# Optimization experiments

Hardware: AMD Instinct MI355X
Metric: run time of the kernel (lower is better)

## Reference

```python
import jax, jax.numpy as jnp
import numpy as np

N = 32768          # nodes
E = 131072         # edges
H = 4              # heads
RNA = 128          # rna_feature_dim
PROT = 32          # prot_feature_dim
F0 = 64            # num_features_per_layer[0] == [1]
CIN = F0 + PROT    # cross-path feature dim (96)
LRELU = 0.2


def _param(key, shape):
    return jax.random.normal(key, shape, dtype=jnp.float32) * 0.1


def setup_inputs() -> dict:
    key = jax.random.key(0)
    ks = jax.random.split(key, 20)
    return {
        "rna_data": jax.random.normal(ks[0], (N, RNA), dtype=jnp.float32),
        "prot_data": jax.random.normal(ks[1], (N, PROT), dtype=jnp.float32),
        "edge_index": jax.random.randint(ks[2], (2, E), 0, N, dtype=jnp.int32),
        "W_gat_proj": _param(ks[3], (RNA, F0)),
        "b_gat_proj": _param(ks[4], (F0,)),
        "W_gat_reproj": _param(ks[5], (F0, RNA)),
        "b_gat_reproj": _param(ks[6], (RNA,)),
        "Wg": _param(ks[7], (F0, H * F0)),
        "ag_src": _param(ks[8], (H, F0)),
        "ag_trg": _param(ks[9], (H, F0)),
        "bg": _param(ks[10], (F0,)),
        "W_cross_proj": _param(ks[11], (RNA + PROT, CIN)),
        "b_cross_proj": _param(ks[12], (CIN,)),
        "W_cross_reproj": _param(ks[13], (CIN, RNA + PROT)),
        "b_cross_reproj": _param(ks[14], (RNA + PROT,)),
        "Wc": _param(ks[15], (CIN, H * CIN)),
        "ac_src": _param(ks[16], (H, CIN)),
        "ac_trg": _param(ks[17], (H, CIN)),
        "bc": _param(ks[18], (CIN,)),
    }


def gat_layer(x, W, a_src, a_trg, bias, edge_index, softmax_on_src):
    """GATLayer with concat=False, activation=None, skip connection (in==out dim),
    dropout in eval mode. CrossAttnLayer groups the edge-softmax by src instead of trg."""
    n, f = x.shape
    src, trg = edge_index[0], edge_index[1]
    proj = (x @ W).reshape(n, H, f)                               # [N,H,F] lift targets
    s_src = jnp.einsum('nhf,hf->nh', proj, a_src)                 # [N,H]
    s_trg = jnp.einsum('nhf,hf->nh', proj, a_trg)                 # [N,H]
    scores = jax.nn.leaky_relu(s_src[src] + s_trg[trg], LRELU)    # [E,H] per-edge scores
    grp = src if softmax_on_src else trg
    ex = jnp.exp(scores - scores.max())                           # global-max shift (as in source)
    denom = jax.ops.segment_sum(ex, grp, num_segments=n)          # [N,H]
    attn = ex / (denom[grp] + 1e-16)                              # neighborhood-aware softmax [E,H]
    weighted = proj[src] * attn[:, :, None]                       # [E,H,F]
    out = jax.ops.segment_sum(weighted, trg, num_segments=n)      # scatter-add aggregate [N,H,F]
    out = out + x[:, None, :]                                     # direct skip (out_dim == in_dim)
    out = out.mean(axis=1) + bias                                 # concat=False -> head mean, + bias
    return out                                                    # activation=None (last layer)


def reference(rna_data, prot_data, edge_index,
              W_gat_proj, b_gat_proj, W_gat_reproj, b_gat_reproj,
              Wg, ag_src, ag_trg, bg,
              W_cross_proj, b_cross_proj, W_cross_reproj, b_cross_reproj,
              Wc, ac_src, ac_trg, bc):
    concat = jnp.concatenate([rna_data, prot_data], axis=1)       # [N, RNA+PROT]
    rna_p = rna_data @ W_gat_proj + b_gat_proj                    # [N, F0]
    cross_p = concat @ W_cross_proj + b_cross_proj                # [N, CIN]
    gat_out = gat_layer(rna_p, Wg, ag_src, ag_trg, bg, edge_index, False)    # [N, F0]
    cross_out = gat_layer(cross_p, Wc, ac_src, ac_trg, bc, edge_index, True)  # [N, CIN]
    # CrossAttnLayer's trailing view(-1, num_heads, num_out_features)
    cross_out = cross_out.reshape(-1, H, CIN)                     # [N/H, H, CIN]
    gat_final = gat_out @ W_gat_reproj + b_gat_reproj             # [N, RNA]
    cross_final = cross_out @ W_cross_reproj + b_cross_reproj     # [N/H, H, RNA+PROT]
    return gat_final, cross_final
```

## Files before the change

### kernel.cpp

```cpp
#include <hip/hip_runtime.h>
#include <hip/hip_bf16.h>

#define NN 32768
#define NE 131072
#define HH 4

constexpr float kLrelu = 0.2f;

using bf16x8 = __attribute__((ext_vector_type(8))) __bf16;
using f32x4  = __attribute__((ext_vector_type(4))) float;

__device__ inline short f2b(float f) {
    __hip_bfloat16 h = __float2bfloat16(f);
    return __builtin_bit_cast(short, h);
}
__device__ inline float b2f(short s) {
    __hip_bfloat16 h = __builtin_bit_cast(__hip_bfloat16, s);
    return __bfloat162float(h);
}
__device__ inline float blo(int u) {
    return __builtin_bit_cast(float, (int)(u << 16));
}
__device__ inline float bhi(int u) {
    return __builtin_bit_cast(float, (int)(u & 0xffff0000));
}
__device__ inline float lrexp(float x) {
    return __expf(x > 0.f ? x : kLrelu * x);
}

template<int K, int LDA, int OUTN, int BM, int BN, bool BF16OUT>
__global__ __launch_bounds__(256) void mfma_gemm(
    const short* __restrict__ A, const short* __restrict__ Wt,
    const float* __restrict__ bias,
    float* __restrict__ Cf, short* __restrict__ Cb)
{
    constexpr int KP    = K + 8;
    constexpr int WM    = BM / 32;
    constexpr int WN    = 4 / WM;
    constexpr int WBN   = BN / WN;
    constexpr int CF    = WBN / 16;
    constexpr int CPR   = K / 8;
    constexpr int TOT   = (BM + BN) * KP;
    constexpr int SLICE = TOT / 4;

    __shared__ short lds[TOT];
    short* As = lds;
    short* Bs = lds + BM * KP;

    const int tid  = threadIdx.x;
    const int wave = tid >> 6;
    const int lane = tid & 63;
    const int lr   = lane & 15;
    const int kb   = lane >> 4;
    const int wm   = wave % WM;
    const int wn   = wave / WM;
    const int row0 = blockIdx.x * BM;
    const int col0 = blockIdx.y * BN;

    #pragma unroll
    for (int g = tid; g < BM * CPR; g += 256) {
        int r = g / CPR, c = g - r * CPR;
        bf16x8 v = *(const bf16x8*)(A + (size_t)(row0 + r) * LDA + c * 8);
        *(bf16x8*)(As + r * KP + c * 8) = v;
    }
    #pragma unroll
    for (int g = tid; g < BN * CPR; g += 256) {
        int r = g / CPR, c = g - r * CPR;
        bf16x8 v = *(const bf16x8*)(Wt + (size_t)(col0 + r) * K + c * 8);
        *(bf16x8*)(Bs + r * KP + c * 8) = v;
    }
    __syncthreads();

    f32x4 acc[2][CF] = {};
    #pragma unroll
    for (int k0 = 0; k0 < K; k0 += 32) {
        bf16x8 af0 = *(const bf16x8*)(As + (wm * 32 + lr     ) * KP + k0 + kb * 8);
        bf16x8 af1 = *(const bf16x8*)(As + (wm * 32 + lr + 16) * KP + k0 + kb * 8);
        #pragma unroll
        for (int cf = 0; cf < CF; ++cf) {
            bf16x8 bv = *(const bf16x8*)(Bs + (wn * WBN + cf * 16 + lr) * KP + k0 + kb * 8);
            acc[0][cf] = __builtin_amdgcn_mfma_f32_16x16x32_bf16(af0, bv, acc[0][cf], 0, 0, 0);
            acc[1][cf] = __builtin_amdgcn_mfma_f32_16x16x32_bf16(af1, bv, acc[1][cf], 0, 0, 0);
        }
    }

    #pragma unroll
    for (int mf = 0; mf < 2; ++mf) {
        __syncthreads();
        if constexpr (BF16OUT) {
            constexpr int LEP = WBN + 8;
            short* ep = lds + wave * SLICE;
            #pragma unroll
            for (int cf = 0; cf < CF; ++cf) {
                const int c  = cf * 16 + lr;
                const float bv = bias ? bias[col0 + wn * WBN + c] : 0.0f;
                #pragma unroll
                for (int j = 0; j < 4; ++j)
                    ep[(kb * 4 + j) * LEP + c] = f2b(acc[mf][cf][j] + bv);
            }
            __syncthreads();
            constexpr int CROW = WBN / 8;
            for (int g = lane; g < 16 * CROW; g += 64) {
                int r = g / CROW, cc = g - r * CROW;
                bf16x8 v = *(const bf16x8*)(ep + r * LEP + cc * 8);
                *(bf16x8*)(Cb + (size_t)(row0 + wm * 32 + mf * 16 + r) * OUTN
                              + col0 + wn * WBN + cc * 8) = v;
            }
        } else {
            constexpr int LEPF = WBN + 4;
            float* epf = (float*)(lds + wave * SLICE);
            #pragma unroll
            for (int cf = 0; cf < CF; ++cf) {
                const int c  = cf * 16 + lr;
                const float bv = bias ? bias[col0 + wn * WBN + c] : 0.0f;
                #pragma unroll
                for (int j = 0; j < 4; ++j)
                    epf[(kb * 4 + j) * LEPF + c] = acc[mf][cf][j] + bv;
            }
            __syncthreads();
            constexpr int CROWF = WBN / 4;
            for (int g = lane; g < 16 * CROWF; g += 64) {
                int r = g / CROWF, cc = g - r * CROWF;
                float4 v = *(const float4*)(epf + r * LEPF + cc * 4);
                *(float4*)(Cf + (size_t)(row0 + wm * 32 + mf * 16 + r) * OUTN
                              + col0 + wn * WBN + cc * 4) = v;
            }
        }
    }
}

template<int F>
__global__ __launch_bounds__(256) void scores_proj(
    const short* __restrict__ proj_b,
    const float* __restrict__ a_src, const float* __restrict__ a_trg,
    float* __restrict__ ssrc, float* __restrict__ strg)
{
    int t = blockIdx.x * 256 + threadIdx.x;
    if (t >= NN * HH) return;
    int n = t >> 2, h = t & 3;
    const int4* p = (const int4*)(proj_b + (size_t)n * (4 * F) + h * F);
    const float* as = a_src + h * F;
    const float* at = a_trg + h * F;
    float ss = 0.f, st = 0.f;
    #pragma unroll
    for (int c = 0; c < F / 8; ++c) {
        int4 v = p[c];
        int u[4] = { v.x, v.y, v.z, v.w };
        #pragma unroll
        for (int q = 0; q < 4; ++q) {
            float x0 = blo(u[q]), x1 = bhi(u[q]);
            ss += x0 * as[c * 8 + 2 * q] + x1 * as[c * 8 + 2 * q + 1];
            st += x0 * at[c * 8 + 2 * q] + x1 * at[c * 8 + 2 * q + 1];
        }
    }
    ssrc[t] = ss;
    strg[t] = st;
}

__global__ __launch_bounds__(256) void prep_kernel(
    const float* __restrict__ rna, const float* __restrict__ prot,
    short* __restrict__ cb,
    const float* W0, const float* W1, const float* W2,
    const float* W3, const float* W4, const float* W5,
    short* T0, short* T1, short* T2, short* T3, short* T4, short* T5,
    int4* __restrict__ zero_p)
{
    const int bid = blockIdx.x;
    if (bid < 5120) {
        int t = bid * 256 + threadIdx.x;
        int n = t / 40, j = (t - n * 40) * 4;
        float4 v = (j < 128) ? *(const float4*)(rna  + (size_t)n * 128 + j)
                             : *(const float4*)(prot + (size_t)n * 32 + (j - 128));
        short4 o = { f2b(v.x), f2b(v.y), f2b(v.z), f2b(v.w) };
        *(short4*)(cb + (size_t)n * 160 + j) = o;
    } else if (bid < 5984) {
        int idx = bid - 5120;
        int wsel = idx / 144, sub = idx - wsel * 144;
        int K, N; const float* W; short* T;
        switch (wsel) {
            case 0: K = 128; N =  64; W = W0; T = T0; break;
            case 1: K =  64; N = 256; W = W1; T = T1; break;
            case 2: K =  64; N = 128; W = W2; T = T2; break;
            case 3: K = 160; N =  96; W = W3; T = T3; break;
            case 4: K =  96; N = 384; W = W4; T = T4; break;
            default:K =  96; N = 160; W = W5; T = T5; break;
        }
        int t = sub * 256 + threadIdx.x;
        if (t >= K * N) return;
        int n = t / K, k = t - n * K;
        T[t] = f2b(W[(size_t)k * N + n]);
    } else {
        zero_p[(bid - 5984) * 256 + threadIdx.x] = make_int4(0, 0, 0, 0);
    }
}

__global__ __launch_bounds__(256) void hist_dual(const int* __restrict__ ei,
                                                 int* __restrict__ deg_t,
                                                 int* __restrict__ deg_s)
{
    int e = blockIdx.x * 256 + threadIdx.x;
    if (e >= NE) return;
    atomicAdd(&deg_s[ei[e]], 1);
    atomicAdd(&deg_t[ei[NE + e]], 1);
}

__global__ __launch_bounds__(1024) void scan_dual(
    const int* __restrict__ deg_t, int* __restrict__ rowptr_t, int* __restrict__ cursor_t,
    const int* __restrict__ deg_s, int* __restrict__ rowptr_s, int* __restrict__ cursor_s)
{
    const int* deg    = blockIdx.x ? deg_s    : deg_t;
    int*       rowptr = blockIdx.x ? rowptr_s : rowptr_t;
    int*       cursor = blockIdx.x ? cursor_s : cursor_t;
    __shared__ int sums[1024];
    const int t = threadIdx.x;
    const int base = t * 32;
    int local[32];
    int s = 0;
    #pragma unroll
    for (int i = 0; i < 32; ++i) { local[i] = s; s += deg[base + i]; }
    sums[t] = s;
    __syncthreads();
    for (int off = 1; off < 1024; off <<= 1) {
        int v = (t >= off) ? sums[t - off] : 0;
        __syncthreads();
        sums[t] += v;
        __syncthreads();
    }
    const int prev = (t == 0) ? 0 : sums[t - 1];
    #pragma unroll
    for (int i = 0; i < 32; ++i) {
        rowptr[base + i] = prev + local[i];
        cursor[base + i] = prev + local[i];
    }
    if (t == 1023) rowptr[NN] = prev + s;
}

__global__ __launch_bounds__(256) void scatter_dual(
    const int* __restrict__ ei,
    int* __restrict__ cursor_t, int* __restrict__ csr_srcT,
    int* __restrict__ cursor_s, int* __restrict__ csr_trgS)
{
    int e = blockIdx.x * 256 + threadIdx.x;
    if (e >= NE) return;
    int s = ei[e], t = ei[NE + e];
    int st = atomicAdd(&cursor_t[t], 1);
    csr_srcT[st] = s;
    int ss = atomicAdd(&cursor_s[s], 1);
    csr_trgS[ss] = t;
}

__global__ __launch_bounds__(256) void den_src_kernel(
    const int* __restrict__ rowptr_s, const int* __restrict__ csr_trgS,
    const float* __restrict__ ssrc, const float* __restrict__ strg,
    float* __restrict__ recip)
{
    int n = blockIdx.x * 256 + threadIdx.x;
    if (n >= NN) return;
    const int beg = rowptr_s[n], end = rowptr_s[n + 1];
    const float4 sv = *(const float4*)(ssrc + 4 * (size_t)n);
    float d0 = 0.f, d1 = 0.f, d2 = 0.f, d3 = 0.f;
    for (int sl = beg; sl < end; ++sl) {
        const int t = csr_trgS[sl];
        const float4 tv = *(const float4*)(strg + 4 * (size_t)t);
        d0 += lrexp(sv.x + tv.x); d1 += lrexp(sv.y + tv.y);
        d2 += lrexp(sv.z + tv.z); d3 += lrexp(sv.w + tv.w);
    }
    *(float4*)(recip + 4 * (size_t)n) =
        make_float4(1.f / (d0 + 1e-16f), 1.f / (d1 + 1e-16f),
                    1.f / (d2 + 1e-16f), 1.f / (d3 + 1e-16f));
}

template<int F, int NPB, bool GROUP_SRC>
__global__ __launch_bounds__((F / 2) * NPB) void aggregate_fused(
    const int* __restrict__ rowptr_t, const int* __restrict__ csr_srcT,
    const float* __restrict__ ssrc, const float* __restrict__ strg,
    const float* __restrict__ recip,
    const short* __restrict__ proj_b,
    const short* __restrict__ x_pb, const float* __restrict__ bias,
    short* __restrict__ aggb)
{
    const int f2   = threadIdx.x * 2;
    const int node = blockIdx.x * NPB + threadIdx.y;
    const int beg  = rowptr_t[node], end = rowptr_t[node + 1];
    const float4 stv = *(const float4*)(strg + 4 * (size_t)node);

    float a0 = 0.f, a1 = 0.f;
    float h0l = 0.f, h1l = 0.f, h2l = 0.f, h3l = 0.f;
    float h0h = 0.f, h1h = 0.f, h2h = 0.f, h3h = 0.f;
    float d0 = 0.f, d1 = 0.f, d2 = 0.f, d3 = 0.f;

    #pragma unroll 2
    for (int sl = beg; sl < end; ++sl) {
        const int s = csr_srcT[sl];
        const float4 sv = *(const float4*)(ssrc + 4 * (size_t)s);
        float e0 = lrexp(sv.x + stv.x);
        float e1 = lrexp(sv.y + stv.y);
        float e2 = lrexp(sv.z + stv.z);
        float e3 = lrexp(sv.w + stv.w);
        const short* p = proj_b + (size_t)s * (4 * F) + f2;
        const int u0 = *(const int*)(p);
        const int u1 = *(const int*)(p + F);
        const int u2 = *(const int*)(p + 2 * F);
        const int u3 = *(const int*)(p + 3 * F);
        if constexpr (GROUP_SRC) {
            const float4 rc = *(const float4*)(recip + 4 * (size_t)s);
            e0 *= rc.x; e1 *= rc.y; e2 *= rc.z; e3 *= rc.w;
            a0 += e0 * blo(u0) + e1 * blo(u1) + e2 * blo(u2) + e3 * blo(u3);
            a1 += e0 * bhi(u0) + e1 * bhi(u1) + e2 * bhi(u2) + e3 * bhi(u3);
        } else {
            d0 += e0; d1 += e1; d2 += e2; d3 += e3;
            h0l += e0 * blo(u0); h0h += e0 * bhi(u0);
            h1l += e1 * blo(u1); h1h += e1 * bhi(u1);
            h2l += e2 * blo(u2); h2h += e2 * bhi(u2);
            h3l += e3 * blo(u3); h3h += e3 * bhi(u3);
        }
    }
    if constexpr (!GROUP_SRC) {
        const float r0 = 1.f / (d0 + 1e-16f), r1 = 1.f / (d1 + 1e-16f);
        const float r2 = 1.f / (d2 + 1e-16f), r3 = 1.f / (d3 + 1e-16f);
        a0 = h0l * r0 + h1l * r1 + h2l * r2 + h3l * r3;
        a1 = h0h * r0 + h1h * r1 + h2h * r2 + h3h * r3;
    }
    const int o = node * F + f2;
    const int ux = *(const int*)(x_pb + o);
    const float v0 = a0 * 0.25f + blo(ux) + bias[f2];
    const float v1 = a1 * 0.25f + bhi(ux) + bias[f2 + 1];
    const int packed = (f2b(v0) & 0xffff) | ((int)f2b(v1) << 16);
    *(int*)(aggb + o) = packed;
}

extern "C" void kernel_launch(void* const* d_in, const int* in_sizes, int n_in,
                              void* d_out, int out_size, void* d_ws, size_t ws_size,
                              hipStream_t stream)
{
    const float* rna   = (const float*)d_in[0];
    const float* prot  = (const float*)d_in[1];
    const int*   ei    = (const int*)  d_in[2];
    const float* Wgp   = (const float*)d_in[3];
    const float* bgp   = (const float*)d_in[4];
    const float* Wgr   = (const float*)d_in[5];
    const float* bgr   = (const float*)d_in[6];
    const float* Wg    = (const float*)d_in[7];
    const float* ags   = (const float*)d_in[8];
    const float* agt   = (const float*)d_in[9];
    const float* bg    = (const float*)d_in[10];
    const float* Wcp   = (const float*)d_in[11];
    const float* bcp   = (const float*)d_in[12];
    const float* Wcr   = (const float*)d_in[13];
    const float* bcr   = (const float*)d_in[14];
    const float* Wc    = (const float*)d_in[15];
    const float* acs   = (const float*)d_in[16];
    const float* act   = (const float*)d_in[17];
    const float* bc    = (const float*)d_in[18];

    float* out_gat   = (float*)d_out;
    float* out_cross = out_gat + (size_t)NN * 128;

    float* ssrc   = (float*)d_ws;
    float* strg   = ssrc + (size_t)NN * 4;
    float* recip  = strg + (size_t)NN * 4;
    short* proj_b = (short*)(recip + (size_t)NN * 4);
    short* cb     = proj_b + (size_t)NN * 384;
    short* x_pb   = cb    + (size_t)NN * 160;
    short* aggb   = x_pb  + (size_t)NN * 96;
    short* wt_gp  = aggb  + (size_t)NN * 96;
    short* wt_g   = wt_gp + 128 * 64;
    short* wt_gr  = wt_g  + 64 * 256;
    short* wt_cp  = wt_gr + 64 * 128;
    short* wt_c   = wt_cp + 160 * 96;
    short* wt_cr  = wt_c  + 96 * 384;
    int*   deg_t  = (int*)(wt_cr + 96 * 160);
    int*   deg_s  = deg_t  + NN;
    int*   cursor_t = deg_s  + NN;
    int*   cursor_s = cursor_t + NN;
    int*   rowptr_t = cursor_s + NN;
    int*   rowptr_s = rowptr_t + NN + 1;
    int*   csr_srcT = rowptr_s + NN + 1;
    int*   csr_trgS = csr_srcT + NE;

    prep_kernel<<<6048, 256, 0, stream>>>(rna, prot, cb,
                                          Wgp, Wg, Wgr, Wcp, Wc, Wcr,
                                          wt_gp, wt_g, wt_gr, wt_cp, wt_c, wt_cr,
                                          (int4*)deg_t);
    hist_dual<<<NE / 256, 256, 0, stream>>>(ei, deg_t, deg_s);
    scan_dual<<<2, 1024, 0, stream>>>(deg_t, rowptr_t, cursor_t, deg_s, rowptr_s, cursor_s);
    scatter_dual<<<NE / 256, 256, 0, stream>>>(ei, cursor_t, csr_srcT, cursor_s, csr_trgS);

    mfma_gemm<128, 160,  64, 32,  64, true ><<<dim3(1024, 1), 256, 0, stream>>>(cb,   wt_gp, bgp, nullptr, x_pb);
    mfma_gemm< 64,  64, 256, 64, 128, true ><<<dim3( 512, 2), 256, 0, stream>>>(x_pb, wt_g,  nullptr, nullptr, proj_b);
    scores_proj<64><<<(NN * HH) / 256, 256, 0, stream>>>(proj_b, ags, agt, ssrc, strg);
    aggregate_fused<64, 8, false><<<NN / 8, dim3(32, 8), 0, stream>>>(
        rowptr_t, csr_srcT, ssrc, strg, nullptr, proj_b, x_pb, bg, aggb);
    mfma_gemm< 64,  64, 128, 64,  64, false><<<dim3( 512, 2), 256, 0, stream>>>(aggb, wt_gr, bgr, out_gat, nullptr);

    mfma_gemm<160, 160,  96, 64,  96, true ><<<dim3( 512, 1), 256, 0, stream>>>(cb,   wt_cp, bcp, nullptr, x_pb);
    mfma_gemm< 96,  96, 384, 64, 128, true ><<<dim3( 512, 3), 256, 0, stream>>>(x_pb, wt_c,  nullptr, nullptr, proj_b);
    scores_proj<96><<<(NN * HH) / 256, 256, 0, stream>>>(proj_b, acs, act, ssrc, strg);
    den_src_kernel<<<NN / 256, 256, 0, stream>>>(rowptr_s, csr_trgS, ssrc, strg, recip);
    aggregate_fused<96, 8, true><<<NN / 8, dim3(48, 8), 0, stream>>>(
        rowptr_t, csr_srcT, ssrc, strg, recip, proj_b, x_pb, bc, aggb);
    mfma_gemm< 96,  96, 160, 64, 160, false><<<dim3( 512, 1), 256, 0, stream>>>(aggb, wt_cr, bcr, out_cross, nullptr);
}
```

Before: 178.1 us.

## Fuse GAT and cross-attention score and aggregation kernels into joint launches

Gives the two attention paths separate workspace buffers so they can run together. The two score kernels become one launch, and the two aggregation kernels become one launch that walks the trg-CSR edge list once for both paths. In the joint aggregation, the first 32 threads of each 48-wide row also handle the GAT path. This saves launches and one pass over the edge indices and gathers, at the cost of extra workspace, higher register pressure, and idle lanes for the GAT half.

```diff
diff --git a/kernel.cpp b/kernel.cpp
--- a/kernel.cpp
+++ b/kernel.cpp
@@ -130,13 +130,11 @@
 }
 
 template<int F>
-__global__ __launch_bounds__(256) void scores_proj(
+__device__ inline void score_one(
     const short* __restrict__ proj_b,
     const float* __restrict__ a_src, const float* __restrict__ a_trg,
-    float* __restrict__ ssrc, float* __restrict__ strg)
-{
-    int t = blockIdx.x * 256 + threadIdx.x;
-    if (t >= NN * HH) return;
+    float* __restrict__ ssrc, float* __restrict__ strg, int t)
+{
     int n = t >> 2, h = t & 3;
     const int4* p = (const int4*)(proj_b + (size_t)n * (4 * F) + h * F);
     const float* as = a_src + h * F;
@@ -155,6 +153,19 @@
     }
     ssrc[t] = ss;
     strg[t] = st;
+}
+
+__global__ __launch_bounds__(256) void scores_both(
+    const short* __restrict__ projG,
+    const float* __restrict__ agsG, const float* __restrict__ agtG,
+    float* __restrict__ ssrcG, float* __restrict__ strgG,
+    const short* __restrict__ projC,
+    const float* __restrict__ acsC, const float* __restrict__ actC,
+    float* __restrict__ ssrcC, float* __restrict__ strgC)
+{
+    int t = blockIdx.x * 256 + threadIdx.x;
+    if (t < NN * HH) score_one<64>(projG, agsG, agtG, ssrcG, strgG, t);
+    else             score_one<96>(projC, acsC, actC, ssrcC, strgC, t - NN * HH);
 }
 
 __global__ __launch_bounds__(256) void prep_kernel(
@@ -270,63 +281,83 @@
                     1.f / (d2 + 1e-16f), 1.f / (d3 + 1e-16f));
 }
 
-template<int F, int NPB, bool GROUP_SRC>
-__global__ __launch_bounds__((F / 2) * NPB) void aggregate_fused(
+template<int NPB>
+__global__ __launch_bounds__(48 * NPB) void aggregate_both(
     const int* __restrict__ rowptr_t, const int* __restrict__ csr_srcT,
-    const float* __restrict__ ssrc, const float* __restrict__ strg,
+    const float* __restrict__ ssrcG, const float* __restrict__ strgG,
+    const float* __restrict__ ssrcC, const float* __restrict__ strgC,
     const float* __restrict__ recip,
-    const short* __restrict__ proj_b,
-    const short* __restrict__ x_pb, const float* __restrict__ bias,
-    short* __restrict__ aggb)
-{
-    const int f2   = threadIdx.x * 2;
+    const short* __restrict__ projG, const short* __restrict__ projC,
+    const short* __restrict__ xG, const short* __restrict__ xC,
+    const float* __restrict__ biasG, const float* __restrict__ biasC,
+    short* __restrict__ aggG, short* __restrict__ aggC)
+{
+    const int fx   = threadIdx.x;
+    const int f2   = fx * 2;
+    const bool doG = fx < 32;
     const int node = blockIdx.x * NPB + threadIdx.y;
     const int beg  = rowptr_t[node], end = rowptr_t[node + 1];
-    const float4 stv = *(const float4*)(strg + 4 * (size_t)node);
-
-    float a0 = 0.f, a1 = 0.f;
-    float h0l = 0.f, h1l = 0.f, h2l = 0.f, h3l = 0.f;
-    float h0h = 0.f, h1h = 0.f, h2h = 0.f, h3h = 0.f;
+    const float4 stC = *(const float4*)(strgC + 4 * (size_t)node);
+    const float4 stG = *(const float4*)(strgG + 4 * (size_t)node);
+
+    float c0 = 0.f, c1 = 0.f;
+    float g0l = 0.f, g1l = 0.f, g2l = 0.f, g3l = 0.f;
+    float g0h = 0.f, g1h = 0.f, g2h = 0.f, g3h = 0.f;
     float d0 = 0.f, d1 = 0.f, d2 = 0.f, d3 = 0.f;
 
-    #pragma unroll 2
+    #pragma unroll 4
     for (int sl = beg; sl < end; ++sl) {
         const int s = csr_srcT[sl];
-        const float4 sv = *(const float4*)(ssrc + 4 * (size_t)s);
-        float e0 = lrexp(sv.x + stv.x);
-        float e1 = lrexp(sv.y + stv.y);
-        float e2 = lrexp(sv.z + stv.z);
-        float e3 = lrexp(sv.w + stv.w);
-        const short* p = proj_b + (size_t)s * (4 * F) + f2;
-        const int u0 = *(const int*)(p);
-        const int u1 = *(const int*)(p + F);
-        const int u2 = *(const int*)(p + 2 * F);
-        const int u3 = *(const int*)(p + 3 * F);
-        if constexpr (GROUP_SRC) {
-            const float4 rc = *(const float4*)(recip + 4 * (size_t)s);
-            e0 *= rc.x; e1 *= rc.y; e2 *= rc.z; e3 *= rc.w;
-            a0 += e0 * blo(u0) + e1 * blo(u1) + e2 * blo(u2) + e3 * blo(u3);
-            a1 += e0 * bhi(u0) + e1 * bhi(u1) + e2 * bhi(u2) + e3 * bhi(u3);
-        } else {
-            d0 += e0; d1 += e1; d2 += e2; d3 += e3;
-            h0l += e0 * blo(u0); h0h += e0 * bhi(u0);
-            h1l += e1 * blo(u1); h1h += e1 * bhi(u1);
-            h2l += e2 * blo(u2); h2h += e2 * bhi(u2);
-            h3l += e3 * blo(u3); h3h += e3 * bhi(u3);
+        const float4 svC = *(const float4*)(ssrcC + 4 * (size_t)s);
+        const float4 rc  = *(const float4*)(recip + 4 * (size_t)s);
+        const short* pC = projC + (size_t)s * 384 + f2;
+        const int uc0 = *(const int*)(pC);
+        const int uc1 = *(const int*)(pC + 96);
+        const int uc2 = *(const int*)(pC + 192);
+        const int uc3 = *(const int*)(pC + 288);
+        const float e0 = lrexp(svC.x + stC.x) * rc.x;
+        const float e1 = lrexp(svC.y + stC.y) * rc.y;
+        const float e2 = lrexp(svC.z + stC.z) * rc.z;
+        const float e3 = lrexp(svC.w + stC.w) * rc.w;
+        c0 += e0 * blo(uc0) + e1 * blo(uc1) + e2 * blo(uc2) + e3 * blo(uc3);
+        c1 += e0 * bhi(uc0) + e1 * bhi(uc1) + e2 * bhi(uc2) + e3 * bhi(uc3);
+        if (doG) {
+            const float4 svG = *(const float4*)(ssrcG + 4 * (size_t)s);
+            const short* pG = projG + (size_t)s * 256 + f2;
+            const int ug0 = *(const int*)(pG);
+            const int ug1 = *(const int*)(pG + 64);
+            const int ug2 = *(const int*)(pG + 128);
+            const int ug3 = *(const int*)(pG + 192);
+            const float q0 = lrexp(svG.x + stG.x);
+            const float q1 = lrexp(svG.y + stG.y);
+            const float q2 = lrexp(svG.z + stG.z);
+            const float q3 = lrexp(svG.w + stG.w);
+            d0 += q0; d1 += q1; d2 += q2; d3 += q3;
+            g0l += q0 * blo(ug0); g0h += q0 * bhi(ug0);
+            g1l += q1 * blo(ug1); g1h += q1 * bhi(ug1);
+            g2l += q2 * blo(ug2); g2h += q2 * bhi(ug2);
+            g3l += q3 * blo(ug3); g3h += q3 * bhi(ug3);
         }
     }
-    if constexpr (!GROUP_SRC) {
+
+    {
+        const int o = node * 96 + f2;
+        const int ux = *(const int*)(xC + o);
+        const float v0 = c0 * 0.25f + blo(ux) + biasC[f2];
+        const float v1 = c1 * 0.25f + bhi(ux) + biasC[f2 + 1];
+        *(int*)(aggC + o) = (f2b(v0) & 0xffff) | ((int)f2b(v1) << 16);
+    }
+    if (doG) {
         const float r0 = 1.f / (d0 + 1e-16f), r1 = 1.f / (d1 + 1e-16f);
         const float r2 = 1.f / (d2 + 1e-16f), r3 = 1.f / (d3 + 1e-16f);
-        a0 = h0l * r0 + h1l * r1 + h2l * r2 + h3l * r3;
-        a1 = h0h * r0 + h1h * r1 + h2h * r2 + h3h * r3;
-    }
-    const int o = node * F + f2;
-    const int ux = *(const int*)(x_pb + o);
-    const float v0 = a0 * 0.25f + blo(ux) + bias[f2];
-    const float v1 = a1 * 0.25f + bhi(ux) + bias[f2 + 1];
-    const int packed = (f2b(v0) & 0xffff) | ((int)f2b(v1) << 16);
-    *(int*)(aggb + o) = packed;
+        const float a0 = g0l * r0 + g1l * r1 + g2l * r2 + g3l * r3;
+        const float a1 = g0h * r0 + g1h * r1 + g2h * r2 + g3h * r3;
+        const int o = node * 64 + f2;
+        const int ux = *(const int*)(xG + o);
+        const float v0 = a0 * 0.25f + blo(ux) + biasG[f2];
+        const float v1 = a1 * 0.25f + bhi(ux) + biasG[f2 + 1];
+        *(int*)(aggG + o) = (f2b(v0) & 0xffff) | ((int)f2b(v1) << 16);
+    }
 }
 
 extern "C" void kernel_launch(void* const* d_in, const int* in_sizes, int n_in,
@@ -356,14 +387,19 @@
     float* out_gat   = (float*)d_out;
     float* out_cross = out_gat + (size_t)NN * 128;
 
-    float* ssrc   = (float*)d_ws;
-    float* strg   = ssrc + (size_t)NN * 4;
-    float* recip  = strg + (size_t)NN * 4;
-    short* proj_b = (short*)(recip + (size_t)NN * 4);
-    short* cb     = proj_b + (size_t)NN * 384;
-    short* x_pb   = cb    + (size_t)NN * 160;
-    short* aggb   = x_pb  + (size_t)NN * 96;
-    short* wt_gp  = aggb  + (size_t)NN * 96;
+    float* ssrcG  = (float*)d_ws;
+    float* strgG  = ssrcG + (size_t)NN * 4;
+    float* ssrcC  = strgG + (size_t)NN * 4;
+    float* strgC  = ssrcC + (size_t)NN * 4;
+    float* recip  = strgC + (size_t)NN * 4;
+    short* projG  = (short*)(recip + (size_t)NN * 4);
+    short* projC  = projG + (size_t)NN * 256;
+    short* cb     = projC + (size_t)NN * 384;
+    short* x_pG   = cb    + (size_t)NN * 160;
+    short* x_pC   = x_pG  + (size_t)NN * 64;
+    short* aggG   = x_pC  + (size_t)NN * 96;
+    short* aggC   = aggG  + (size_t)NN * 64;
+    short* wt_gp  = aggC  + (size_t)NN * 96;
     short* wt_g   = wt_gp + 128 * 64;
     short* wt_gr  = wt_g  + 64 * 256;
     short* wt_cp  = wt_gr + 64 * 128;
@@ -386,18 +422,18 @@
     scan_dual<<<2, 1024, 0, stream>>>(deg_t, rowptr_t, cursor_t, deg_s, rowptr_s, cursor_s);
     scatter_dual<<<NE / 256, 256, 0, stream>>>(ei, cursor_t, csr_srcT, cursor_s, csr_trgS);
 
-    mfma_gemm<128, 160,  64, 32,  64, true ><<<dim3(1024, 1), 256, 0, stream>>>(cb,   wt_gp, bgp, nullptr, x_pb);
-    mfma_gemm< 64,  64, 256, 64, 128, true ><<<dim3( 512, 2), 256, 0, stream>>>(x_pb, wt_g,  nullptr, nullptr, proj_b);
-    scores_proj<64><<<(NN * HH) / 256, 256, 0, stream>>>(proj_b, ags, agt, ssrc, strg);
-    aggregate_fused<64, 8, false><<<NN / 8, dim3(32, 8), 0, stream>>>(
-        rowptr_t, csr_srcT, ssrc, strg, nullptr, proj_b, x_pb, bg, aggb);
-    mfma_gemm< 64,  64, 128, 64,  64, false><<<dim3( 512, 2), 256, 0, stream>>>(aggb, wt_gr, bgr, out_gat, nullptr);
-
-    mfma_gemm<160, 160,  96, 64,  96, true ><<<dim3( 512, 1), 256, 0, stream>>>(cb,   wt_cp, bcp, nullptr, x_pb);
-    mfma_gemm< 96,  96, 384, 64, 128, true ><<<dim3( 512, 3), 256, 0, stream>>>(x_pb, wt_c,  nullptr, nullptr, proj_b);
-    scores_proj<96><<<(NN * HH) / 256, 256, 0, stream>>>(proj_b, acs, act, ssrc, strg);
-    den_src_kernel<<<NN / 256, 256, 0, stream>>>(rowptr_s, csr_trgS, ssrc, strg, recip);
-    aggregate_fused<96, 8, true><<<NN / 8, dim3(48, 8), 0, stream>>>(
-        rowptr_t, csr_srcT, ssrc, strg, recip, proj_b, x_pb, bc, aggb);
-    mfma_gemm< 96,  96, 160, 64, 160, false><<<dim3( 512, 1), 256, 0, stream>>>(aggb, wt_cr, bcr, out_cross, nullptr);
-}
+    mfma_gemm<128, 160,  64, 32,  64, true ><<<dim3(1024, 1), 256, 0, stream>>>(cb,   wt_gp, bgp, nullptr, x_pG);
+    mfma_gemm<160, 160,  96, 64,  96, true ><<<dim3( 512, 1), 256, 0, stream>>>(cb,   wt_cp, bcp, nullptr, x_pC);
+    mfma_gemm< 64,  64, 256, 64, 128, true ><<<dim3( 512, 2), 256, 0, stream>>>(x_pG, wt_g,  nullptr, nullptr, projG);
+    mfma_gemm< 96,  96, 384, 64, 128, true ><<<dim3( 512, 3), 256, 0, stream>>>(x_pC, wt_c,  nullptr, nullptr, projC);
+
+    scores_both<<<(2 * NN * HH) / 256, 256, 0, stream>>>(
+        projG, ags, agt, ssrcG, strgG, projC, acs, act, ssrcC, strgC);
+    den_src_kernel<<<NN / 256, 256, 0, stream>>>(rowptr_s, csr_trgS, ssrcC, strgC, recip);
+    aggregate_both<8><<<NN / 8, dim3(48, 8), 0, stream>>>(
+        rowptr_t, csr_srcT, ssrcG, strgG, ssrcC, strgC, recip,
+        projG, projC, x_pG, x_pC, bg, bc, aggG, aggC);
+
+    mfma_gemm< 64,  64, 128, 64,  64, false><<<dim3(512, 2), 256, 0, stream>>>(aggG, wt_gr, bgr, out_gat, nullptr);
+    mfma_gemm< 96,  96, 160, 64, 160, false><<<dim3(512, 1), 256, 0, stream>>>(aggC, wt_cr, bcr, out_cross, nullptr);
+}
```

After: 200.0 us. +12.3%, slower.
